# Kernel optimization log

Measured on AMD Instinct MI355X. Metric: run time of the kernel, lower is better.

The kernel has to match this reference:

```python
import jax, jax.numpy as jnp
import numpy as np

B, N, E = 2, 50000, 400000
FIN, HID, OUT = 128, 128, 128
EPS = 1e-5  # BatchNorm1d default eps


def setup_inputs() -> dict:
    key = jax.random.key(0)
    ks = jax.random.split(key, 12)
    x = jax.random.normal(ks[0], (B, N, FIN), dtype=jnp.float32)
    row = jax.random.randint(ks[1], (E,), 0, N, dtype=jnp.int32)          # scatter dst
    col = jnp.concatenate([jnp.arange(N, dtype=jnp.int32),                # ensure deg>=1
                           jax.random.randint(ks[2], (E - N,), 0, N, dtype=jnp.int32)])
    edge_index = jnp.stack([row, col])                                    # [2, E]
    deg = jnp.zeros((N,), jnp.float32).at[col].add(1.0)                   # degree(col, N)
    dis = deg ** -0.5
    norm = (dis[row] * dis[col])[None, :, None]                           # [1, E, 1]
    W1 = jax.random.normal(ks[3], (HID, FIN), jnp.float32) / np.sqrt(FIN)
    b1 = jax.random.normal(ks[4], (HID,), jnp.float32) * 0.01
    g1 = jnp.ones((N,), jnp.float32)
    be1 = jnp.zeros((N,), jnp.float32)
    W2 = jax.random.normal(ks[5], (OUT, HID), jnp.float32) / np.sqrt(HID)
    b2 = jax.random.normal(ks[6], (OUT,), jnp.float32) * 0.01
    g2 = jnp.ones((N,), jnp.float32)
    be2 = jnp.zeros((N,), jnp.float32)
    return {"x": x, "edge_index": edge_index, "norm": norm,
            "W1": W1, "b1": b1, "g1": g1, "be1": be1,
            "W2": W2, "b2": b2, "g2": g2, "be2": be2}


def _gcn_layer(x, edge_index, norm, W, b, g, be):
    # Linear (dropout p=0 -> identity)
    h = jnp.einsum('bnf,of->bno', x, W) + b                 # [B, N, C]
    # BatchNorm1d(num_features=N): per-node stats over (batch, channel)
    mu = jnp.mean(h, axis=(0, 2), keepdims=True)            # [1, N, 1]
    var = jnp.var(h, axis=(0, 2), keepdims=True)            # biased, as torch
    y = g[None, :, None] * (h - mu) * jax.lax.rsqrt(var + EPS) + be[None, :, None]
    a = jax.nn.gelu(y, approximate=False)                   # torch GELU = exact erf
    # message passing: gather src nodes, scale by norm, scatter-add to dst
    msgs = a[:, edge_index[1], :] * norm                    # [B, E, C]
    return jnp.zeros_like(a).at[:, edge_index[0], :].add(msgs)


def reference(x, edge_index, norm, W1, b1, g1, be1, W2, b2, g2, be2):
    x = _gcn_layer(x, edge_index, norm, W1, b1, g1, be1)
    x = _gcn_layer(x, edge_index, norm, W2, b2, g2, be2)
    return x
```

## Files before the change

### kernel.cpp

```cpp
#include <hip/hip_runtime.h>
#include <math.h>

#define CC 128
#define TPAD 132

typedef unsigned short u16;
typedef short bf16x8 __attribute__((ext_vector_type(8)));
typedef short bf16x4 __attribute__((ext_vector_type(4)));
typedef float f32x4 __attribute__((ext_vector_type(4)));

typedef __attribute__((address_space(3))) void lds_t;
typedef const __attribute__((address_space(1))) void gbl_t;

__device__ __forceinline__ u16 f2bf(float f) {
    union { float f; unsigned u; } v; v.f = f;
    unsigned u = v.u;
    return (u16)((u + 0x7FFFu + ((u >> 16) & 1u)) >> 16);
}
__device__ __forceinline__ float bf2f(unsigned hi16) {
    union { unsigned u; float f; } v; v.u = hi16 << 16; return v.f;
}

__device__ __forceinline__ float gelu_f(float y) {
    float xa = fabsf(y) * 0.70710678118654752f;
    float t  = __builtin_amdgcn_rcpf(fmaf(0.3275911f, xa, 1.0f));
    float p  = fmaf(1.061405429f, t, -1.453152027f);
    p = fmaf(p, t, 1.421413741f);
    p = fmaf(p, t, -0.284496736f);
    p = fmaf(p, t, 0.254829592f);
    p *= t;
    float e  = __expf(-xa * xa);
    float er = fmaf(-p, e, 1.0f);
    float s  = copysignf(er, y);
    return 0.5f * y * (1.0f + s);
}


__global__ __launch_bounds__(256) void k_zero_i32(int* __restrict__ p, int n) {
    int i = blockIdx.x * 256 + threadIdx.x;
    if (i < n) p[i] = 0;
}

__global__ __launch_bounds__(256) void k_hist(const int* __restrict__ row, int* __restrict__ cnt, int E) {
    int e = blockIdx.x * 256 + threadIdx.x;
    if (e < E) atomicAdd(&cnt[row[e]], 1);
}

__device__ __forceinline__ int wave_incl_scan(int v) {
    #pragma unroll
    for (int d = 1; d < 64; d <<= 1) {
        int t = __shfl_up(v, d);
        if ((threadIdx.x & 63) >= d) v += t;
    }
    return v;
}

__global__ __launch_bounds__(256) void k_scan_a(const int* __restrict__ cnt, int* __restrict__ bsum, int N) {
    int base = blockIdx.x * 1024 + threadIdx.x * 4;
    int s = 0;
    #pragma unroll
    for (int u = 0; u < 4; ++u) { int i = base + u; if (i < N) s += cnt[i]; }
    #pragma unroll
    for (int d = 32; d > 0; d >>= 1) s += __shfl_down(s, d);
    __shared__ int wsum[4];
    if ((threadIdx.x & 63) == 0) wsum[threadIdx.x >> 6] = s;
    __syncthreads();
    if (threadIdx.x == 0) bsum[blockIdx.x] = wsum[0] + wsum[1] + wsum[2] + wsum[3];
}

__global__ __launch_bounds__(64) void k_scan_b(const int* __restrict__ bsum, int* __restrict__ boff,
                                               int* __restrict__ off, int N, int nb) {
    int carry = 0;
    for (int base = 0; base < nb; base += 64) {
        int t = base + (int)threadIdx.x;
        int v = (t < nb) ? bsum[t] : 0;
        int incl = wave_incl_scan(v);
        if (t < nb) boff[t] = carry + incl - v;
        carry += __shfl(incl, 63);
    }
    if (threadIdx.x == 0) off[N] = carry;
}

__global__ __launch_bounds__(256) void k_scan_c(int* __restrict__ cnt, const int* __restrict__ boff,
                                                int* __restrict__ off, int N) {
    int t = threadIdx.x;
    int base = blockIdx.x * 1024 + t * 4;
    int v[4]; int s = 0;
    #pragma unroll
    for (int u = 0; u < 4; ++u) { int i = base + u; v[u] = (i < N) ? cnt[i] : 0; s += v[u]; }
    int incl = wave_incl_scan(s);
    __shared__ int wsum[4];
    int w = t >> 6, lane = t & 63;
    if (lane == 63) wsum[w] = incl;
    __syncthreads();
    int run = incl - s + boff[blockIdx.x];
    for (int ww = 0; ww < w; ++ww) run += wsum[ww];
    #pragma unroll
    for (int u = 0; u < 4; ++u) {
        int i = base + u;
        if (i < N) { off[i] = run; cnt[i] = 0; }
        run += v[u];
    }
}

__global__ __launch_bounds__(256) void k_fill(const int* __restrict__ row, const int* __restrict__ col,
                                              const float* __restrict__ nrm, const int* __restrict__ off,
                                              int* __restrict__ cur, int2* __restrict__ eg, int E) {
    int e = blockIdx.x * 256 + threadIdx.x;
    if (e < E) {
        int r = row[e];
        int p = off[r] + atomicAdd(&cur[r], 1);
        eg[p] = make_int2(col[e], __float_as_int(nrm[e]));
    }
}

__global__ __launch_bounds__(256) void k_wrepack(const float* __restrict__ W1, u16* __restrict__ Wp1,
                                                 const float* __restrict__ W2, u16* __restrict__ Wp2) {
    int i = blockIdx.x * 256 + threadIdx.x;
    const float* W = (i < CC * CC) ? W1 : W2;
    u16* Wp = (i < CC * CC) ? Wp1 : Wp2;
    int ii = (i < CC * CC) ? i : i - CC * CC;
    if (ii < CC * CC) {
        int j = ii & 7, l = (ii >> 3) & 63, s = (ii >> 9) & 3, t = ii >> 11;
        int r = 16 * t + (l & 15);
        int k = s * 32 + (l >> 4) * 8 + j;
        Wp[ii] = f2bf(W[r * CC + k]);
    }
}

template<int IN_BF16>
__global__ __launch_bounds__(256, 4) void k_gemm_bn_gelu(
    const void* __restrict__ Xv, const u16* __restrict__ Wp,
    const float* __restrict__ bias, const float* __restrict__ gamma, const float* __restrict__ beta,
    u16* __restrict__ Out, int N)
{
    __shared__ __align__(16) u16 SM[CC * CC];

    const int tid = threadIdx.x;
    const int w = tid >> 6;
    const int l = tid & 63;
    const int g = l >> 4;
    const int c = l & 15;
    const int n8 = blockIdx.x * 32 + w * 8;
    const bool valid = n8 < N;
    const int nbase = valid ? n8 : 0;

    #pragma unroll
    for (int it = 0; it < 8; ++it) {
        const u16* gsrc = Wp + it * 2048 + w * 512 + l * 8;
        u16* ldst = &SM[it * 2048 + w * 512];
        __builtin_amdgcn_global_load_lds((gbl_t*)gsrc, (lds_t*)ldst, 16, 0, 0);
    }

    const int ab = c >> 3;
    const int an = nbase + (c & 7);

    bf16x8 af[4];
    if (IN_BF16) {
        const u16* X = (const u16*)Xv;
        const u16* base = X + ((size_t)ab * N + an) * CC + g * 8;
        #pragma unroll
        for (int s = 0; s < 4; ++s) af[s] = *(const bf16x8*)(base + s * 32);
    } else {
        const float* X = (const float*)Xv;
        const float* base = X + ((size_t)ab * N + an) * CC + g * 8;
        float4 lo[4], hi[4];
        #pragma unroll
        for (int s = 0; s < 4; ++s) {
            lo[s] = *(const float4*)(base + s * 32);
            hi[s] = *(const float4*)(base + s * 32 + 4);
        }
        #pragma unroll
        for (int s = 0; s < 4; ++s) {
            bf16x8 v;
            v[0] = (short)f2bf(lo[s].x); v[1] = (short)f2bf(lo[s].y);
            v[2] = (short)f2bf(lo[s].z); v[3] = (short)f2bf(lo[s].w);
            v[4] = (short)f2bf(hi[s].x); v[5] = (short)f2bf(hi[s].y);
            v[6] = (short)f2bf(hi[s].z); v[7] = (short)f2bf(hi[s].w);
            af[s] = v;
        }
    }

    float bb[8];
    #pragma unroll
    for (int t = 0; t < 8; ++t) bb[t] = bias[t * 16 + c];
    float gam[4], bet[4];
    #pragma unroll
    for (int r = 0; r < 4; ++r) {
        int p = (4 * g + r) & 7;
        gam[r] = gamma[nbase + p];
        bet[r] = beta[nbase + p];
    }

    __syncthreads();

    f32x4 acc[8];
    #pragma unroll
    for (int t = 0; t < 8; ++t) acc[t] = (f32x4){0.f, 0.f, 0.f, 0.f};

    #pragma unroll
    for (int s = 0; s < 4; ++s) {
        bf16x8 bf[8];
        #pragma unroll
        for (int t = 0; t < 8; ++t)
            bf[t] = *(const bf16x8*)&SM[((t * 4 + s) * 64 + l) * 8];
        #pragma unroll
        for (int t = 0; t < 8; ++t)
            acc[t] = __builtin_amdgcn_mfma_f32_16x16x32_bf16(af[s], bf[t], acc[t], 0, 0, 0);
    }

    float rs[4] = {0.f, 0.f, 0.f, 0.f}, rq[4] = {0.f, 0.f, 0.f, 0.f};
    #pragma unroll
    for (int t = 0; t < 8; ++t)
        #pragma unroll
        for (int r = 0; r < 4; ++r) {
            float h = acc[t][r] + bb[t];
            acc[t][r] = h;
            rs[r] += h;
            rq[r] += h * h;
        }
    #pragma unroll
    for (int d = 1; d < 16; d <<= 1) {
        #pragma unroll
        for (int r = 0; r < 4; ++r) {
            rs[r] += __shfl_xor(rs[r], d);
            rq[r] += __shfl_xor(rq[r], d);
        }
    }
    #pragma unroll
    for (int r = 0; r < 4; ++r) {
        rs[r] += __shfl_xor(rs[r], 32);
        rq[r] += __shfl_xor(rq[r], 32);
    }

    float sc[4], sh[4];
    #pragma unroll
    for (int r = 0; r < 4; ++r) {
        float mean = rs[r] * (1.f / 256.f);
        float var  = rq[r] * (1.f / 256.f) - mean * mean;
        float s_ = gam[r] * rsqrtf(fmaxf(var, 0.f) + 1e-5f);
        sc[r] = s_;
        sh[r] = bet[r] - mean * s_;
    }

    __syncthreads();

    u16 (*T)[TPAD] = (u16 (*)[TPAD])(SM + w * 16 * TPAD);
    #pragma unroll
    for (int r = 0; r < 4; ++r) {
        int row = 4 * g + r;
        #pragma unroll
        for (int t = 0; t < 8; ++t) {
            float y = acc[t][r] * sc[r] + sh[r];
            T[row][t * 16 + c] = f2bf(gelu_f(y));
        }
    }

    if (valid) {
        #pragma unroll
        for (int it = 0; it < 4; ++it) {
            int chunk = it * 64 + l;
            int rowi = chunk >> 4;
            int offc = (chunk & 15) * 8;
            int db = rowi >> 3;
            int dn = n8 + (rowi & 7);
            bf16x4 lo = *(const bf16x4*)&T[rowi][offc];
            bf16x4 hi = *(const bf16x4*)&T[rowi][offc + 4];
            bf16x8 v;
            v[0] = lo[0]; v[1] = lo[1]; v[2] = lo[2]; v[3] = lo[3];
            v[4] = hi[0]; v[5] = hi[1]; v[6] = hi[2]; v[7] = hi[3];
            *(bf16x8*)(Out + ((size_t)db * N + dn) * CC + offc) = v;
        }
    }
}

template<int OUT_F32>
__global__ __launch_bounds__(256) void k_aggregate(
    const u16* __restrict__ A, const int* __restrict__ off,
    const int2* __restrict__ eg, void* __restrict__ Outv, int N)
{
    int n = blockIdx.x * 4 + (threadIdx.x >> 6);
    if (n >= N) return;
    int l = threadIdx.x & 63;
    int p = l >> 5;
    int b = (l >> 4) & 1;
    int ch0 = (l & 15) * 8;
    const u16* Ab = A + (size_t)b * N * CC + ch0;
    int s = off[n], e = off[n + 1];
    float a[8] = {0.f, 0.f, 0.f, 0.f, 0.f, 0.f, 0.f, 0.f};
    for (int j = s; j < e; j += 8) {
        int i0 = j + p, i1 = j + 2 + p, i2 = j + 4 + p, i3 = j + 6 + p;
        int2 e0 = (i0 < e) ? eg[i0] : make_int2(0, 0);
        int2 e1 = (i1 < e) ? eg[i1] : make_int2(0, 0);
        int2 e2 = (i2 < e) ? eg[i2] : make_int2(0, 0);
        int2 e3 = (i3 < e) ? eg[i3] : make_int2(0, 0);
        bf16x8 v0 = *(const bf16x8*)(Ab + (size_t)e0.x * CC);
        bf16x8 v1 = *(const bf16x8*)(Ab + (size_t)e1.x * CC);
        bf16x8 v2 = *(const bf16x8*)(Ab + (size_t)e2.x * CC);
        bf16x8 v3 = *(const bf16x8*)(Ab + (size_t)e3.x * CC);
        float w0 = __int_as_float(e0.y), w1 = __int_as_float(e1.y);
        float w2 = __int_as_float(e2.y), w3 = __int_as_float(e3.y);
        #pragma unroll
        for (int q = 0; q < 8; ++q) {
            a[q] = fmaf(w0, bf2f((u16)v0[q]), a[q]);
            a[q] = fmaf(w1, bf2f((u16)v1[q]), a[q]);
            a[q] = fmaf(w2, bf2f((u16)v2[q]), a[q]);
            a[q] = fmaf(w3, bf2f((u16)v3[q]), a[q]);
        }
    }
    #pragma unroll
    for (int q = 0; q < 8; ++q) a[q] += __shfl_xor(a[q], 32);
    if (l < 32) {
        if (OUT_F32) {
            float* d = (float*)Outv + ((size_t)b * N + n) * CC + ch0;
            *(float4*)&d[0] = make_float4(a[0], a[1], a[2], a[3]);
            *(float4*)&d[4] = make_float4(a[4], a[5], a[6], a[7]);
        } else {
            u16* d = (u16*)Outv + ((size_t)b * N + n) * CC + ch0;
            bf16x8 v;
            #pragma unroll
            for (int q = 0; q < 8; ++q) v[q] = (short)f2bf(a[q]);
            *(bf16x8*)d = v;
        }
    }
}


extern "C" void kernel_launch(void* const* d_in, const int* in_sizes, int n_in,
                              void* d_out, int out_size, void* d_ws, size_t ws_size,
                              hipStream_t stream)
{
    const float* x   = (const float*)d_in[0];
    const int*   ei  = (const int*)d_in[1];
    const float* nrm = (const float*)d_in[2];
    const float* W1  = (const float*)d_in[3];
    const float* b1  = (const float*)d_in[4];
    const float* g1  = (const float*)d_in[5];
    const float* be1 = (const float*)d_in[6];
    const float* W2  = (const float*)d_in[7];
    const float* b2  = (const float*)d_in[8];
    const float* g2  = (const float*)d_in[9];
    const float* be2 = (const float*)d_in[10];

    const int N = in_sizes[5];
    const int E = in_sizes[2];
    const int* row = ei;
    const int* col = ei + E;
    const int nb = (N + 1023) / 1024;

    auto al = [](size_t v) { return (v + 255) & ~(size_t)255; };
    char* p = (char*)d_ws;
    int* off    = (int*)p;   p += al((size_t)(N + 1) * 4);
    int* cur    = (int*)p;   p += al((size_t)N * 4);
    int2* eg    = (int2*)p;  p += al((size_t)E * 8);
    int* bsum   = (int*)p;   p += al((size_t)nb * 4);
    int* boff   = (int*)p;   p += al((size_t)nb * 4);
    u16* Wp1    = (u16*)p;   p += al((size_t)CC * CC * 2);
    u16* Wp2    = (u16*)p;   p += al((size_t)CC * CC * 2);
    u16* bufA   = (u16*)p;   p += al((size_t)2 * N * CC * 2);
    u16* bufB   = (u16*)p;   p += al((size_t)2 * N * CC * 2);

    k_zero_i32<<<(N + 255) / 256, 256, 0, stream>>>(cur, N);
    k_hist<<<(E + 255) / 256, 256, 0, stream>>>(row, cur, E);
    k_scan_a<<<nb, 256, 0, stream>>>(cur, bsum, N);
    k_scan_b<<<1, 64, 0, stream>>>(bsum, boff, off, N, nb);
    k_scan_c<<<nb, 256, 0, stream>>>(cur, boff, off, N);
    k_fill<<<(E + 255) / 256, 256, 0, stream>>>(row, col, nrm, off, cur, eg, E);

    k_wrepack<<<(2 * CC * CC + 255) / 256, 256, 0, stream>>>(W1, Wp1, W2, Wp2);

    const int gb = (N + 31) / 32;
    const int ga = (N + 3) / 4;
    k_gemm_bn_gelu<0><<<gb, 256, 0, stream>>>(x, Wp1, b1, g1, be1, bufA, N);
    k_aggregate<0><<<ga, 256, 0, stream>>>(bufA, off, eg, bufB, N);
    k_gemm_bn_gelu<1><<<gb, 256, 0, stream>>>(bufB, Wp2, b2, g2, be2, bufA, N);
    k_aggregate<1><<<ga, 256, 0, stream>>>(bufA, off, eg, (float*)d_out, N);
}
```

Baseline: 169.9 us.

## Reorder layer-2 linear before aggregation and fuse GEMMs into one kernel

Uses linearity to apply W2 before the first scatter-aggregation, so aggregation then linear becomes linear then aggregation. This lets layer 1's GEMM, BN, GELU and the W2 GEMM run in one kernel, with the intermediate kept in LDS. Layer-2 bias, BatchNorm and GELU are folded into the first aggregation kernel, which removes a full kernel launch and one global round-trip of the intermediate activation. It also uses packed bf16 conversion instructions, adds a permuted W2 layout and a register-resident second MFMA pass, and drops the 4-wave occupancy hint on the GEMM kernel.

```diff
diff --git a/kernel.cpp b/kernel.cpp
--- a/kernel.cpp
+++ b/kernel.cpp
@@ -2,11 +2,9 @@
 #include <math.h>
 
 #define CC 128
-#define TPAD 132
 
 typedef unsigned short u16;
 typedef short bf16x8 __attribute__((ext_vector_type(8)));
-typedef short bf16x4 __attribute__((ext_vector_type(4)));
 typedef float f32x4 __attribute__((ext_vector_type(4)));
 
 typedef __attribute__((address_space(3))) void lds_t;
@@ -19,6 +17,11 @@
 }
 __device__ __forceinline__ float bf2f(unsigned hi16) {
     union { unsigned u; float f; } v; v.u = hi16 << 16; return v.f;
+}
+__device__ __forceinline__ unsigned cvt_pk(float lo, float hi) {
+    unsigned r;
+    asm("v_cvt_pk_bf16_f32 %0, %1, %2" : "=v"(r) : "v"(lo), "v"(hi));
+    return r;
 }
 
 __device__ __forceinline__ float gelu_f(float y) {
@@ -117,24 +120,28 @@
 __global__ __launch_bounds__(256) void k_wrepack(const float* __restrict__ W1, u16* __restrict__ Wp1,
                                                  const float* __restrict__ W2, u16* __restrict__ Wp2) {
     int i = blockIdx.x * 256 + threadIdx.x;
-    const float* W = (i < CC * CC) ? W1 : W2;
-    u16* Wp = (i < CC * CC) ? Wp1 : Wp2;
-    int ii = (i < CC * CC) ? i : i - CC * CC;
-    if (ii < CC * CC) {
+    if (i < 2 * CC * CC) {
+        int is2 = (i >= CC * CC);
+        int ii = is2 ? i - CC * CC : i;
         int j = ii & 7, l = (ii >> 3) & 63, s = (ii >> 9) & 3, t = ii >> 11;
         int r = 16 * t + (l & 15);
-        int k = s * 32 + (l >> 4) * 8 + j;
-        Wp[ii] = f2bf(W[r * CC + k]);
-    }
-}
-
-template<int IN_BF16>
-__global__ __launch_bounds__(256, 4) void k_gemm_bn_gelu(
-    const void* __restrict__ Xv, const u16* __restrict__ Wp,
+        int p = s * 32 + ((l >> 4) & 3) * 8 + j;
+        if (is2) {
+            int k = (p & 7) * 16 + (p >> 3);
+            Wp2[ii] = f2bf(W2[r * CC + k]);
+        } else {
+            Wp1[ii] = f2bf(W1[r * CC + p]);
+        }
+    }
+}
+
+__global__ __launch_bounds__(256) void k_fused_l1(
+    const float* __restrict__ X, const u16* __restrict__ Wp1, const u16* __restrict__ Wp2,
     const float* __restrict__ bias, const float* __restrict__ gamma, const float* __restrict__ beta,
-    u16* __restrict__ Out, int N)
+    u16* __restrict__ Z, int N)
 {
-    __shared__ __align__(16) u16 SM[CC * CC];
+    __shared__ __align__(16) u16 WS[CC * CC];
+    __shared__ __align__(16) unsigned TT[4][16][68];
 
     const int tid = threadIdx.x;
     const int w = tid >> 6;
@@ -147,38 +154,23 @@
 
     #pragma unroll
     for (int it = 0; it < 8; ++it) {
-        const u16* gsrc = Wp + it * 2048 + w * 512 + l * 8;
-        u16* ldst = &SM[it * 2048 + w * 512];
+        const u16* gsrc = Wp1 + it * 2048 + w * 512 + l * 8;
+        u16* ldst = &WS[it * 2048 + w * 512];
         __builtin_amdgcn_global_load_lds((gbl_t*)gsrc, (lds_t*)ldst, 16, 0, 0);
     }
 
     const int ab = c >> 3;
     const int an = nbase + (c & 7);
-
+    const float* xbase = X + ((size_t)ab * N + an) * CC + g * 8;
     bf16x8 af[4];
-    if (IN_BF16) {
-        const u16* X = (const u16*)Xv;
-        const u16* base = X + ((size_t)ab * N + an) * CC + g * 8;
-        #pragma unroll
-        for (int s = 0; s < 4; ++s) af[s] = *(const bf16x8*)(base + s * 32);
-    } else {
-        const float* X = (const float*)Xv;
-        const float* base = X + ((size_t)ab * N + an) * CC + g * 8;
-        float4 lo[4], hi[4];
-        #pragma unroll
-        for (int s = 0; s < 4; ++s) {
-            lo[s] = *(const float4*)(base + s * 32);
-            hi[s] = *(const float4*)(base + s * 32 + 4);
-        }
-        #pragma unroll
-        for (int s = 0; s < 4; ++s) {
-            bf16x8 v;
-            v[0] = (short)f2bf(lo[s].x); v[1] = (short)f2bf(lo[s].y);
-            v[2] = (short)f2bf(lo[s].z); v[3] = (short)f2bf(lo[s].w);
-            v[4] = (short)f2bf(hi[s].x); v[5] = (short)f2bf(hi[s].y);
-            v[6] = (short)f2bf(hi[s].z); v[7] = (short)f2bf(hi[s].w);
-            af[s] = v;
-        }
+    #pragma unroll
+    for (int s = 0; s < 4; ++s) {
+        float4 lo = *(const float4*)(xbase + s * 32);
+        float4 hi = *(const float4*)(xbase + s * 32 + 4);
+        unsigned aw[4];
+        aw[0] = cvt_pk(lo.x, lo.y); aw[1] = cvt_pk(lo.z, lo.w);
+        aw[2] = cvt_pk(hi.x, hi.y); aw[3] = cvt_pk(hi.z, hi.w);
+        af[s] = *(bf16x8*)aw;
     }
 
     float bb[8];
@@ -197,16 +189,24 @@
     f32x4 acc[8];
     #pragma unroll
     for (int t = 0; t < 8; ++t) acc[t] = (f32x4){0.f, 0.f, 0.f, 0.f};
-
     #pragma unroll
     for (int s = 0; s < 4; ++s) {
         bf16x8 bf[8];
         #pragma unroll
         for (int t = 0; t < 8; ++t)
-            bf[t] = *(const bf16x8*)&SM[((t * 4 + s) * 64 + l) * 8];
+            bf[t] = *(const bf16x8*)&WS[((t * 4 + s) * 64 + l) * 8];
         #pragma unroll
         for (int t = 0; t < 8; ++t)
             acc[t] = __builtin_amdgcn_mfma_f32_16x16x32_bf16(af[s], bf[t], acc[t], 0, 0, 0);
+    }
+
+    __syncthreads();
+
+    #pragma unroll
+    for (int it = 0; it < 8; ++it) {
+        const u16* gsrc = Wp2 + it * 2048 + w * 512 + l * 8;
+        u16* ldst = &WS[it * 2048 + w * 512];
+        __builtin_amdgcn_global_load_lds((gbl_t*)gsrc, (lds_t*)ldst, 16, 0, 0);
     }
 
     float rs[4] = {0.f, 0.f, 0.f, 0.f}, rq[4] = {0.f, 0.f, 0.f, 0.f};
@@ -233,59 +233,72 @@
         rq[r] += __shfl_xor(rq[r], 32);
     }
 
-    float sc[4], sh[4];
     #pragma unroll
     for (int r = 0; r < 4; ++r) {
         float mean = rs[r] * (1.f / 256.f);
         float var  = rq[r] * (1.f / 256.f) - mean * mean;
-        float s_ = gam[r] * rsqrtf(fmaxf(var, 0.f) + 1e-5f);
-        sc[r] = s_;
-        sh[r] = bet[r] - mean * s_;
-    }
+        float sc = gam[r] * rsqrtf(fmaxf(var, 0.f) + 1e-5f);
+        float sh = bet[r] - mean * sc;
+        #pragma unroll
+        for (int t = 0; t < 8; ++t)
+            acc[t][r] = gelu_f(acc[t][r] * sc + sh);
+    }
+
+    #pragma unroll
+    for (int r = 0; r < 4; ++r) {
+        unsigned tw[4];
+        #pragma unroll
+        for (int tt = 0; tt < 4; ++tt)
+            tw[tt] = cvt_pk(acc[2 * tt][r], acc[2 * tt + 1][r]);
+        *(uint4*)&TT[w][4 * g + r][c * 4] = *(uint4*)tw;
+    }
+    bf16x8 af2[4];
+    #pragma unroll
+    for (int s = 0; s < 4; ++s)
+        af2[s] = *(const bf16x8*)&TT[w][c][s * 16 + g * 4];
 
     __syncthreads();
 
-    u16 (*T)[TPAD] = (u16 (*)[TPAD])(SM + w * 16 * TPAD);
-    #pragma unroll
-    for (int r = 0; r < 4; ++r) {
-        int row = 4 * g + r;
-        #pragma unroll
-        for (int t = 0; t < 8; ++t) {
-            float y = acc[t][r] * sc[r] + sh[r];
-            T[row][t * 16 + c] = f2bf(gelu_f(y));
-        }
+    f32x4 acc2[8];
+    #pragma unroll
+    for (int t = 0; t < 8; ++t) acc2[t] = (f32x4){0.f, 0.f, 0.f, 0.f};
+    #pragma unroll
+    for (int s = 0; s < 4; ++s) {
+        bf16x8 bf[8];
+        #pragma unroll
+        for (int t = 0; t < 8; ++t)
+            bf[t] = *(const bf16x8*)&WS[((t * 4 + s) * 64 + l) * 8];
+        #pragma unroll
+        for (int t = 0; t < 8; ++t)
+            acc2[t] = __builtin_amdgcn_mfma_f32_16x16x32_bf16(af2[s], bf[t], acc2[t], 0, 0, 0);
     }
 
     if (valid) {
         #pragma unroll
-        for (int it = 0; it < 4; ++it) {
-            int chunk = it * 64 + l;
-            int rowi = chunk >> 4;
-            int offc = (chunk & 15) * 8;
-            int db = rowi >> 3;
-            int dn = n8 + (rowi & 7);
-            bf16x4 lo = *(const bf16x4*)&T[rowi][offc];
-            bf16x4 hi = *(const bf16x4*)&T[rowi][offc + 4];
-            bf16x8 v;
-            v[0] = lo[0]; v[1] = lo[1]; v[2] = lo[2]; v[3] = lo[3];
-            v[4] = hi[0]; v[5] = hi[1]; v[6] = hi[2]; v[7] = hi[3];
-            *(bf16x8*)(Out + ((size_t)db * N + dn) * CC + offc) = v;
-        }
-    }
-}
-
-template<int OUT_F32>
-__global__ __launch_bounds__(256) void k_aggregate(
-    const u16* __restrict__ A, const int* __restrict__ off,
-    const int2* __restrict__ eg, void* __restrict__ Outv, int N)
+        for (int r = 0; r < 4; ++r) {
+            int rr = 4 * g + r;
+            int db = rr >> 3, dn = n8 + (rr & 7);
+            unsigned zw[4];
+            #pragma unroll
+            for (int tt = 0; tt < 4; ++tt)
+                zw[tt] = cvt_pk(acc2[2 * tt][r], acc2[2 * tt + 1][r]);
+            *(uint4*)(Z + ((size_t)db * N + dn) * CC + c * 8) = *(uint4*)zw;
+        }
+    }
+}
+
+__global__ __launch_bounds__(256) void k_agg_bn(
+    const u16* __restrict__ Zin, const int* __restrict__ off, const int2* __restrict__ eg,
+    const float* __restrict__ b2, const float* __restrict__ g2, const float* __restrict__ be2,
+    u16* __restrict__ A2, int N)
 {
     int n = blockIdx.x * 4 + (threadIdx.x >> 6);
     if (n >= N) return;
     int l = threadIdx.x & 63;
     int p = l >> 5;
     int b = (l >> 4) & 1;
-    int ch0 = (l & 15) * 8;
-    const u16* Ab = A + (size_t)b * N * CC + ch0;
+    int c = l & 15;
+    const u16* Ab = Zin + (size_t)b * N * CC + c * 8;
     int s = off[n], e = off[n + 1];
     float a[8] = {0.f, 0.f, 0.f, 0.f, 0.f, 0.f, 0.f, 0.f};
     for (int j = s; j < e; j += 8) {
@@ -310,18 +323,76 @@
     }
     #pragma unroll
     for (int q = 0; q < 8; ++q) a[q] += __shfl_xor(a[q], 32);
+
+    float ss = 0.f, qq = 0.f;
+    #pragma unroll
+    for (int t = 0; t < 8; ++t) {
+        float h = a[t] + b2[t * 16 + c];
+        a[t] = h;
+        ss += h;
+        qq += h * h;
+    }
+    #pragma unroll
+    for (int d = 1; d < 32; d <<= 1) {
+        ss += __shfl_xor(ss, d);
+        qq += __shfl_xor(qq, d);
+    }
+    float mean = ss * (1.f / 256.f);
+    float var  = qq * (1.f / 256.f) - mean * mean;
+    float sc = g2[n] * rsqrtf(fmaxf(var, 0.f) + 1e-5f);
+    float sh = be2[n] - mean * sc;
+
     if (l < 32) {
-        if (OUT_F32) {
-            float* d = (float*)Outv + ((size_t)b * N + n) * CC + ch0;
-            *(float4*)&d[0] = make_float4(a[0], a[1], a[2], a[3]);
-            *(float4*)&d[4] = make_float4(a[4], a[5], a[6], a[7]);
-        } else {
-            u16* d = (u16*)Outv + ((size_t)b * N + n) * CC + ch0;
-            bf16x8 v;
-            #pragma unroll
-            for (int q = 0; q < 8; ++q) v[q] = (short)f2bf(a[q]);
-            *(bf16x8*)d = v;
-        }
+        unsigned ow[4];
+        #pragma unroll
+        for (int tt = 0; tt < 4; ++tt) {
+            float y0 = gelu_f(a[2 * tt] * sc + sh);
+            float y1 = gelu_f(a[2 * tt + 1] * sc + sh);
+            ow[tt] = cvt_pk(y0, y1);
+        }
+        *(uint4*)(A2 + ((size_t)b * N + n) * CC + c * 8) = *(uint4*)ow;
+    }
+}
+
+__global__ __launch_bounds__(256) void k_agg_out(
+    const u16* __restrict__ A2, const int* __restrict__ off, const int2* __restrict__ eg,
+    float* __restrict__ Out, int N)
+{
+    int n = blockIdx.x * 4 + (threadIdx.x >> 6);
+    if (n >= N) return;
+    int l = threadIdx.x & 63;
+    int p = l >> 5;
+    int b = (l >> 4) & 1;
+    int c = l & 15;
+    const u16* Ab = A2 + (size_t)b * N * CC + c * 8;
+    int s = off[n], e = off[n + 1];
+    float a[8] = {0.f, 0.f, 0.f, 0.f, 0.f, 0.f, 0.f, 0.f};
+    for (int j = s; j < e; j += 8) {
+        int i0 = j + p, i1 = j + 2 + p, i2 = j + 4 + p, i3 = j + 6 + p;
+        int2 e0 = (i0 < e) ? eg[i0] : make_int2(0, 0);
+        int2 e1 = (i1 < e) ? eg[i1] : make_int2(0, 0);
+        int2 e2 = (i2 < e) ? eg[i2] : make_int2(0, 0);
+        int2 e3 = (i3 < e) ? eg[i3] : make_int2(0, 0);
+        bf16x8 v0 = *(const bf16x8*)(Ab + (size_t)e0.x * CC);
+        bf16x8 v1 = *(const bf16x8*)(Ab + (size_t)e1.x * CC);
+        bf16x8 v2 = *(const bf16x8*)(Ab + (size_t)e2.x * CC);
+        bf16x8 v3 = *(const bf16x8*)(Ab + (size_t)e3.x * CC);
+        float w0 = __int_as_float(e0.y), w1 = __int_as_float(e1.y);
+        float w2 = __int_as_float(e2.y), w3 = __int_as_float(e3.y);
+        #pragma unroll
+        for (int q = 0; q < 8; ++q) {
+            a[q] = fmaf(w0, bf2f((u16)v0[q]), a[q]);
+            a[q] = fmaf(w1, bf2f((u16)v1[q]), a[q]);
+            a[q] = fmaf(w2, bf2f((u16)v2[q]), a[q]);
+            a[q] = fmaf(w3, bf2f((u16)v3[q]), a[q]);
+        }
+    }
+    #pragma unroll
+    for (int q = 0; q < 8; ++q) a[q] += __shfl_xor(a[q], 32);
+    if (l < 32) {
+        float* d = Out + ((size_t)b * N + n) * CC + c;
+        #pragma unroll
+        for (int t = 0; t < 8; ++t) d[t * 16] = a[t];
     }
 }
 
@@ -357,8 +428,8 @@
     int* boff   = (int*)p;   p += al((size_t)nb * 4);
     u16* Wp1    = (u16*)p;   p += al((size_t)CC * CC * 2);
     u16* Wp2    = (u16*)p;   p += al((size_t)CC * CC * 2);
-    u16* bufA   = (u16*)p;   p += al((size_t)2 * N * CC * 2);
-    u16* bufB   = (u16*)p;   p += al((size_t)2 * N * CC * 2);
+    u16* Zbuf   = (u16*)p;   p += al((size_t)2 * N * CC * 2);
+    u16* A2buf  = (u16*)p;   p += al((size_t)2 * N * CC * 2);
 
     k_zero_i32<<<(N + 255) / 256, 256, 0, stream>>>(cur, N);
     k_hist<<<(E + 255) / 256, 256, 0, stream>>>(row, cur, E);
@@ -371,8 +442,7 @@
 
     const int gb = (N + 31) / 32;
     const int ga = (N + 3) / 4;
-    k_gemm_bn_gelu<0><<<gb, 256, 0, stream>>>(x, Wp1, b1, g1, be1, bufA, N);
-    k_aggregate<0><<<ga, 256, 0, stream>>>(bufA, off, eg, bufB, N);
-    k_gemm_bn_gelu<1><<<gb, 256, 0, stream>>>(bufB, Wp2, b2, g2, be2, bufA, N);
-    k_aggregate<1><<<ga, 256, 0, stream>>>(bufA, off, eg, (float*)d_out, N);
-}
+    k_fused_l1<<<gb, 256, 0, stream>>>(x, Wp1, Wp2, b1, g1, be1, Zbuf, N);
+    k_agg_bn<<<ga, 256, 0, stream>>>(Zbuf, off, eg, b2, g2, be2, A2buf, N);
+    k_agg_out<<<ga, 256, 0, stream>>>(A2buf, off, eg, (float*)d_out, N);
+}
```

Measured after the change: 160.6 us. 5.5% less time.
